# Optimization experiments

Measured on AMD Instinct MI355X. Metric: run time of the kernel, lower is better.

The kernel has to match this reference:

```python
import jax, jax.numpy as jnp
import numpy as np

WIN = 7                 # skimage default win_size (gaussian_weights=False)
K1, K2 = 0.01, 0.03     # skimage defaults
DATA_RANGE = 2.0        # skimage dtype range for float images: dmax - dmin = 1 - (-1)


def _uniform_filter_valid(x):
    """7x7 uniform (mean) filter, VALID padding, depthwise over channels.
    x: [B, C, H, W] -> [B, C, H-6, W-6]. Equivalent to skimage uniform_filter
    followed by crop(pad) since reflected borders are discarded."""
    C = x.shape[1]
    k = jnp.full((C, 1, WIN, WIN), 1.0 / (WIN * WIN), dtype=x.dtype)
    return jax.lax.conv_general_dilated(
        x, k, window_strides=(1, 1), padding='VALID',
        dimension_numbers=('NCHW', 'OIHW', 'NCHW'),
        feature_group_count=C)


def _ssim_mean(pred, target):
    N = WIN * WIN
    cov_norm = N / (N - 1.0)  # sample covariance (skimage use_sample_covariance=True)
    ux = _uniform_filter_valid(pred)
    uy = _uniform_filter_valid(target)
    uxx = _uniform_filter_valid(pred * pred)
    uyy = _uniform_filter_valid(target * target)
    uxy = _uniform_filter_valid(pred * target)
    vx = cov_norm * (uxx - ux * ux)
    vy = cov_norm * (uyy - uy * uy)
    vxy = cov_norm * (uxy - ux * uy)
    C1 = (K1 * DATA_RANGE) ** 2
    C2 = (K2 * DATA_RANGE) ** 2
    S = ((2.0 * ux * uy + C1) * (2.0 * vxy + C2)) / (
        (ux * ux + uy * uy + C1) * (vx + vy + C2))
    # equal-weight mean over channels / images == global mean of valid map
    return jnp.mean(S)


def setup_inputs() -> dict:
    key = jax.random.key(0)
    k1, k2 = jax.random.split(key)
    shape = (32, 3, 512, 512)
    pred = jax.random.uniform(k1, shape, dtype=jnp.float32)
    target = jax.random.uniform(k2, shape, dtype=jnp.float32)
    return {"pred": pred, "target": target}


def reference(pred, target):
    return 1.0 - _ssim_mean(pred, target)
```

## Files before the change

kernel.cpp:

```cpp
#include <hip/hip_runtime.h>

#define IMG 512
#define VALID 506
#define NPLANES 96
#define BAND_ROWS 64
#define NBANDS 8
#define HSTRIDE 520

__device__ __forceinline__ float ssim_val(const float s[5]) {
    const float inv_n = 1.0f / 49.0f;
    const float cn    = 49.0f / 48.0f;
    const float C1 = 4.0e-4f;
    const float C2 = 3.6e-3f;
    float ux  = s[0] * inv_n;
    float uy  = s[1] * inv_n;
    float uxx = s[2] * inv_n;
    float uyy = s[3] * inv_n;
    float uxy = s[4] * inv_n;
    float vx  = cn * (uxx - ux * ux);
    float vy  = cn * (uyy - uy * uy);
    float vxy = cn * (uxy - ux * uy);
    float num = (2.0f * ux * uy + C1) * (2.0f * vxy + C2);
    float den = (ux * ux + uy * uy + C1) * (vx + vy + C2);
    return __fdividef(num, den);
}

__global__ __launch_bounds__(256) void ssim_slide_kernel(
    const float* __restrict__ pred,
    const float* __restrict__ target,
    double* __restrict__ accum)
{
    __shared__ float hv[2][5][HSTRIDE];
    __shared__ float wsum[4];

    const int band  = blockIdx.x;
    const int plane = blockIdx.y;
    const int t = threadIdx.x;
    const int c = t << 1;
    const int b = band * BAND_ROWS;
    const int n = (VALID - b < BAND_ROWS) ? (VALID - b) : BAND_ROWS;

    const float* __restrict__ px_ptr = pred   + (size_t)plane * (IMG * IMG) + c;
    const float* __restrict__ py_ptr = target + (size_t)plane * (IMG * IMG) + c;

    float2 Vx  = make_float2(0.f, 0.f);
    float2 Vy  = Vx, Vxx = Vx, Vyy = Vx, Vxy = Vx;
    float2 hx[7], hy[7];

    #pragma unroll
    for (int k = 0; k < 6; ++k) {
        float2 px = *reinterpret_cast<const float2*>(px_ptr + (size_t)(b + k) * IMG);
        float2 py = *reinterpret_cast<const float2*>(py_ptr + (size_t)(b + k) * IMG);
        hx[k] = px; hy[k] = py;
        Vx.x  += px.x;        Vx.y  += px.y;
        Vy.x  += py.x;        Vy.y  += py.y;
        Vxx.x += px.x * px.x; Vxx.y += px.y * px.y;
        Vyy.x += py.x * py.x; Vyy.y += py.y * py.y;
        Vxy.x += px.x * py.x; Vxy.y += px.y * py.y;
    }

    float local = 0.f;

    auto row_step = [&](float2& hxs, float2& hys, bool do_sub, int r, int p) {
        float2 px = *reinterpret_cast<const float2*>(px_ptr + (size_t)r * IMG);
        float2 py = *reinterpret_cast<const float2*>(py_ptr + (size_t)r * IMG);
        if (do_sub) {
            float2 ox = hxs, oy = hys;
            Vx.x  -= ox.x;        Vx.y  -= ox.y;
            Vy.x  -= oy.x;        Vy.y  -= oy.y;
            Vxx.x -= ox.x * ox.x; Vxx.y -= ox.y * ox.y;
            Vyy.x -= oy.x * oy.x; Vyy.y -= oy.y * oy.y;
            Vxy.x -= ox.x * oy.x; Vxy.y -= ox.y * oy.y;
        }
        hxs = px; hys = py;
        Vx.x  += px.x;        Vx.y  += px.y;
        Vy.x  += py.x;        Vy.y  += py.y;
        Vxx.x += px.x * px.x; Vxx.y += px.y * px.y;
        Vyy.x += py.x * py.x; Vyy.y += py.y * py.y;
        Vxy.x += px.x * py.x; Vxy.y += px.y * py.y;

        *reinterpret_cast<float2*>(&hv[p][0][c]) = Vx;
        *reinterpret_cast<float2*>(&hv[p][1][c]) = Vy;
        *reinterpret_cast<float2*>(&hv[p][2][c]) = Vxx;
        *reinterpret_cast<float2*>(&hv[p][3][c]) = Vyy;
        *reinterpret_cast<float2*>(&hv[p][4][c]) = Vxy;
        __syncthreads();

        if (c < VALID) {
            float s0[5], s1[5];
            #pragma unroll
            for (int m = 0; m < 5; ++m) {
                const float* row = &hv[p][m][c];
                float2 r0 = *reinterpret_cast<const float2*>(row);
                float2 r1 = *reinterpret_cast<const float2*>(row + 2);
                float2 r2 = *reinterpret_cast<const float2*>(row + 4);
                float2 r3 = *reinterpret_cast<const float2*>(row + 6);
                float a = r0.x + r0.y + r1.x + r1.y + r2.x + r2.y + r3.x;
                s0[m] = a;
                s1[m] = a - r0.x + r3.y;
            }
            local += ssim_val(s0);
            local += ssim_val(s1);
        }
    };

    row_step(hx[6], hy[6], false, b + 6, 0);

    for (int ii = 1; ii < BAND_ROWS; ii += 7) {
        #pragma unroll
        for (int k = 0; k < 7; ++k) {
            const int i = ii + k;
            if (i < n)
                row_step(hx[k], hy[k], true, b + 6 + i, i & 1);
        }
    }

    #pragma unroll
    for (int off = 32; off > 0; off >>= 1)
        local += __shfl_down(local, off, 64);
    if ((t & 63) == 0) wsum[t >> 6] = local;
    __syncthreads();
    if (t == 0)
        atomicAdd(accum, (double)(wsum[0] + wsum[1] + wsum[2] + wsum[3]));
}

__global__ void ssim_finalize_kernel(const double* __restrict__ accum,
                                     float* __restrict__ out)
{
    const double n_valid = (double)NPLANES * (double)VALID * (double)VALID;
    out[0] = (float)(1.0 - accum[0] / n_valid);
}

extern "C" void kernel_launch(void* const* d_in, const int* in_sizes, int n_in,
                              void* d_out, int out_size, void* d_ws, size_t ws_size,
                              hipStream_t stream) {
    const float* pred   = (const float*)d_in[0];
    const float* target = (const float*)d_in[1];
    float* out = (float*)d_out;
    double* accum = (double*)d_ws;

    hipMemsetAsync(d_ws, 0, sizeof(double), stream);

    dim3 grid(NBANDS, NPLANES);
    ssim_slide_kernel<<<grid, 256, 0, stream>>>(pred, target, accum);
    ssim_finalize_kernel<<<1, 1, 0, stream>>>(accum, out);
}
```

Measured before the change: 88.29 us.

## Replace shared-memory horizontal sums with per-wave cross-lane permutes in SSIM

Each wavefront now owns a 16-row band covering a whole 512-column row, with each lane holding 8 columns. The horizontal 7-tap sums are done with ds_bpermute from the neighbouring lane instead of going through shared memory, which removes the per-row __syncthreads. Rows leaving the window are reloaded from global memory rather than kept in registers, and the SSIM formula is rescaled algebraically to avoid the 1/49 multiplies. This adds redundant global reads (an extra 6-row halo per band plus the old-row reloads) in exchange for no block-level barriers and more bands available for parallelism.

Result: faster. 82.53 us (-6.5%).

```diff
diff --git a/kernel.cpp b/kernel.cpp
--- a/kernel.cpp
+++ b/kernel.cpp
@@ -1,124 +1,145 @@
 #include <hip/hip_runtime.h>
 
-#define IMG 512
-#define VALID 506
+#define IMG     512
+#define VALID   506
 #define NPLANES 96
-#define BAND_ROWS 64
-#define NBANDS 8
-#define HSTRIDE 520
+#define R       16
+#define BANDS   32
 
-__device__ __forceinline__ float ssim_val(const float s[5]) {
-    const float inv_n = 1.0f / 49.0f;
-    const float cn    = 49.0f / 48.0f;
-    const float C1 = 4.0e-4f;
-    const float C2 = 3.6e-3f;
-    float ux  = s[0] * inv_n;
-    float uy  = s[1] * inv_n;
-    float uxx = s[2] * inv_n;
-    float uyy = s[3] * inv_n;
-    float uxy = s[4] * inv_n;
-    float vx  = cn * (uxx - ux * ux);
-    float vy  = cn * (uyy - uy * uy);
-    float vxy = cn * (uxy - ux * uy);
-    float num = (2.0f * ux * uy + C1) * (2.0f * vxy + C2);
-    float den = (ux * ux + uy * uy + C1) * (vx + vy + C2);
-    return __fdividef(num, den);
+__device__ __forceinline__ float shfl_next(float v, int baddr) {
+    return __int_as_float(__builtin_amdgcn_ds_bpermute(baddr, __float_as_int(v)));
 }
 
-__global__ __launch_bounds__(256) void ssim_slide_kernel(
+__device__ __forceinline__ void addv(float4& V, const float4 p) {
+    V.x += p.x; V.y += p.y; V.z += p.z; V.w += p.w;
+}
+__device__ __forceinline__ void subv(float4& V, const float4 p) {
+    V.x -= p.x; V.y -= p.y; V.z -= p.z; V.w -= p.w;
+}
+__device__ __forceinline__ void addmul(float4& V, const float4 p, const float4 q) {
+    V.x = fmaf(p.x, q.x, V.x); V.y = fmaf(p.y, q.y, V.y);
+    V.z = fmaf(p.z, q.z, V.z); V.w = fmaf(p.w, q.w, V.w);
+}
+__device__ __forceinline__ void submul(float4& V, const float4 p, const float4 q) {
+    V.x = fmaf(-p.x, q.x, V.x); V.y = fmaf(-p.y, q.y, V.y);
+    V.z = fmaf(-p.z, q.z, V.z); V.w = fmaf(-p.w, q.w, V.w);
+}
+
+__device__ __forceinline__ void hsum7(const float4 A, const float4 B, int baddr, float o[8]) {
+    float n0 = shfl_next(A.x, baddr);
+    float n1 = shfl_next(A.y, baddr);
+    float n2 = shfl_next(A.z, baddr);
+    float n3 = shfl_next(A.w, baddr);
+    float n4 = shfl_next(B.x, baddr);
+    float n5 = shfl_next(B.y, baddr);
+    o[0] = ((A.x + A.y) + (A.z + A.w)) + ((B.x + B.y) + B.z);
+    o[1] = (o[0] - A.x) + B.w;
+    o[2] = (o[1] - A.y) + n0;
+    o[3] = (o[2] - A.z) + n1;
+    o[4] = (o[3] - A.w) + n2;
+    o[5] = (o[4] - B.x) + n3;
+    o[6] = (o[5] - B.y) + n4;
+    o[7] = (o[6] - B.z) + n5;
+}
+
+#define LOADROW(x0, x1, y0, y1, r) do {                                         \
+    const float4* _p = reinterpret_cast<const float4*>(pp + (size_t)(r) * IMG); \
+    const float4* _q = reinterpret_cast<const float4*>(pt + (size_t)(r) * IMG); \
+    x0 = _p[0]; x1 = _p[1]; y0 = _q[0]; y1 = _q[1]; } while (0)
+
+__global__ __launch_bounds__(256, 3) void ssim_wave_kernel(
     const float* __restrict__ pred,
     const float* __restrict__ target,
     double* __restrict__ accum)
 {
-    __shared__ float hv[2][5][HSTRIDE];
     __shared__ float wsum[4];
 
-    const int band  = blockIdx.x;
+    const int t     = threadIdx.x;
+    const int lane  = t & 63;
+    const int wv    = t >> 6;
+    const int band  = blockIdx.x * 4 + wv;
     const int plane = blockIdx.y;
-    const int t = threadIdx.x;
-    const int c = t << 1;
-    const int b = band * BAND_ROWS;
-    const int n = (VALID - b < BAND_ROWS) ? (VALID - b) : BAND_ROWS;
+    const int row0  = band * R;
+    const int col   = lane << 3;
 
-    const float* __restrict__ px_ptr = pred   + (size_t)plane * (IMG * IMG) + c;
-    const float* __restrict__ py_ptr = target + (size_t)plane * (IMG * IMG) + c;
+    const size_t pbase = (size_t)plane * (IMG * IMG);
+    const float* __restrict__ pp = pred   + pbase + col;
+    const float* __restrict__ pt = target + pbase + col;
 
-    float2 Vx  = make_float2(0.f, 0.f);
-    float2 Vy  = Vx, Vxx = Vx, Vyy = Vx, Vxy = Vx;
-    float2 hx[7], hy[7];
+    const int baddr = ((lane + 1) & 63) << 2;
 
-    #pragma unroll
+    float4 z = make_float4(0.f, 0.f, 0.f, 0.f);
+    float4 Vx_a = z, Vx_b = z, Vy_a = z, Vy_b = z;
+    float4 Vxx_a = z, Vxx_b = z, Vyy_a = z, Vyy_b = z, Vxy_a = z, Vxy_b = z;
+
+    float4 nx0, nx1, ny0, ny1;
+    LOADROW(nx0, nx1, ny0, ny1, row0);
+
+    #pragma unroll 2
     for (int k = 0; k < 6; ++k) {
-        float2 px = *reinterpret_cast<const float2*>(px_ptr + (size_t)(b + k) * IMG);
-        float2 py = *reinterpret_cast<const float2*>(py_ptr + (size_t)(b + k) * IMG);
-        hx[k] = px; hy[k] = py;
-        Vx.x  += px.x;        Vx.y  += px.y;
-        Vy.x  += py.x;        Vy.y  += py.y;
-        Vxx.x += px.x * px.x; Vxx.y += px.y * px.y;
-        Vyy.x += py.x * py.x; Vyy.y += py.y * py.y;
-        Vxy.x += px.x * py.x; Vxy.y += px.y * py.y;
+        float4 px0 = nx0, px1 = nx1, py0 = ny0, py1 = ny1;
+        LOADROW(nx0, nx1, ny0, ny1, row0 + k + 1);
+        addv(Vx_a, px0);  addv(Vx_b, px1);
+        addv(Vy_a, py0);  addv(Vy_b, py1);
+        addmul(Vxx_a, px0, px0); addmul(Vxx_b, px1, px1);
+        addmul(Vyy_a, py0, py0); addmul(Vyy_b, py1, py1);
+        addmul(Vxy_a, px0, py0); addmul(Vxy_b, px1, py1);
     }
 
+    const float c1 = 0.9604f;
+    const float c2 = 8.4672f;
     float local = 0.f;
 
-    auto row_step = [&](float2& hxs, float2& hys, bool do_sub, int r, int p) {
-        float2 px = *reinterpret_cast<const float2*>(px_ptr + (size_t)r * IMG);
-        float2 py = *reinterpret_cast<const float2*>(py_ptr + (size_t)r * IMG);
-        if (do_sub) {
-            float2 ox = hxs, oy = hys;
-            Vx.x  -= ox.x;        Vx.y  -= ox.y;
-            Vy.x  -= oy.x;        Vy.y  -= oy.y;
-            Vxx.x -= ox.x * ox.x; Vxx.y -= ox.y * ox.y;
-            Vyy.x -= oy.x * oy.x; Vyy.y -= oy.y * oy.y;
-            Vxy.x -= ox.x * oy.x; Vxy.y -= ox.y * oy.y;
+    #pragma unroll 2
+    for (int i = 0; i < R; ++i) {
+        float4 px0 = nx0, px1 = nx1, py0 = ny0, py1 = ny1;
+
+        float4 ox0, ox1, oy0, oy1;
+        const bool has_old = (i > 0);
+        if (has_old) LOADROW(ox0, ox1, oy0, oy1, row0 + i - 1);
+
+        int rn = row0 + 7 + i; rn = rn < IMG - 1 ? rn : IMG - 1;
+        LOADROW(nx0, nx1, ny0, ny1, rn);
+
+        addv(Vx_a, px0);  addv(Vx_b, px1);
+        addv(Vy_a, py0);  addv(Vy_b, py1);
+        addmul(Vxx_a, px0, px0); addmul(Vxx_b, px1, px1);
+        addmul(Vyy_a, py0, py0); addmul(Vyy_b, py1, py1);
+        addmul(Vxy_a, px0, py0); addmul(Vxy_b, px1, py1);
+        if (has_old) {
+            subv(Vx_a, ox0);  subv(Vx_b, ox1);
+            subv(Vy_a, oy0);  subv(Vy_b, oy1);
+            submul(Vxx_a, ox0, ox0); submul(Vxx_b, ox1, ox1);
+            submul(Vyy_a, oy0, oy0); submul(Vyy_b, oy1, oy1);
+            submul(Vxy_a, ox0, oy0); submul(Vxy_b, ox1, oy1);
         }
-        hxs = px; hys = py;
-        Vx.x  += px.x;        Vx.y  += px.y;
-        Vy.x  += py.x;        Vy.y  += py.y;
-        Vxx.x += px.x * px.x; Vxx.y += px.y * px.y;
-        Vyy.x += py.x * py.x; Vyy.y += py.y * py.y;
-        Vxy.x += px.x * py.x; Vxy.y += px.y * py.y;
 
-        *reinterpret_cast<float2*>(&hv[p][0][c]) = Vx;
-        *reinterpret_cast<float2*>(&hv[p][1][c]) = Vy;
-        *reinterpret_cast<float2*>(&hv[p][2][c]) = Vxx;
-        *reinterpret_cast<float2*>(&hv[p][3][c]) = Vyy;
-        *reinterpret_cast<float2*>(&hv[p][4][c]) = Vxy;
-        __syncthreads();
-
-        if (c < VALID) {
-            float s0[5], s1[5];
+        const bool row_ok = (row0 + i) < VALID;
+        if (row_ok) {
+            float hx[8], hy[8], hxx[8], hyy[8], hxy[8];
+            hsum7(Vx_a,  Vx_b,  baddr, hx);
+            hsum7(Vy_a,  Vy_b,  baddr, hy);
+            hsum7(Vxx_a, Vxx_b, baddr, hxx);
+            hsum7(Vyy_a, Vyy_b, baddr, hyy);
+            hsum7(Vxy_a, Vxy_b, baddr, hxy);
             #pragma unroll
-            for (int m = 0; m < 5; ++m) {
-                const float* row = &hv[p][m][c];
-                float2 r0 = *reinterpret_cast<const float2*>(row);
-                float2 r1 = *reinterpret_cast<const float2*>(row + 2);
-                float2 r2 = *reinterpret_cast<const float2*>(row + 4);
-                float2 r3 = *reinterpret_cast<const float2*>(row + 6);
-                float a = r0.x + r0.y + r1.x + r1.y + r2.x + r2.y + r3.x;
-                s0[m] = a;
-                s1[m] = a - r0.x + r3.y;
+            for (int j = 0; j < 8; ++j) {
+                float t1 = hx[j] * hy[j];
+                float t2 = fmaf(hx[j], hx[j], hy[j] * hy[j]);
+                float n1 = fmaf(2.f, t1, c1);
+                float d1 = t2 + c1;
+                float n2 = fmaf(-2.f, t1, fmaf(98.f, hxy[j], c2));
+                float d2 = fmaf(49.f, hxx[j] + hyy[j], c2) - t2;
+                float S  = __fdividef(n1 * n2, d1 * d2);
+                local += (col + j < VALID) ? S : 0.f;
             }
-            local += ssim_val(s0);
-            local += ssim_val(s1);
-        }
-    };
-
-    row_step(hx[6], hy[6], false, b + 6, 0);
-
-    for (int ii = 1; ii < BAND_ROWS; ii += 7) {
-        #pragma unroll
-        for (int k = 0; k < 7; ++k) {
-            const int i = ii + k;
-            if (i < n)
-                row_step(hx[k], hy[k], true, b + 6 + i, i & 1);
         }
     }
 
     #pragma unroll
     for (int off = 32; off > 0; off >>= 1)
         local += __shfl_down(local, off, 64);
-    if ((t & 63) == 0) wsum[t >> 6] = local;
+    if (lane == 0) wsum[wv] = local;
     __syncthreads();
     if (t == 0)
         atomicAdd(accum, (double)(wsum[0] + wsum[1] + wsum[2] + wsum[3]));
@@ -141,7 +162,7 @@
 
     hipMemsetAsync(d_ws, 0, sizeof(double), stream);
 
-    dim3 grid(NBANDS, NPLANES);
-    ssim_slide_kernel<<<grid, 256, 0, stream>>>(pred, target, accum);
+    dim3 grid(BANDS / 4, NPLANES);
+    ssim_wave_kernel<<<grid, 256, 0, stream>>>(pred, target, accum);
     ssim_finalize_kernel<<<1, 1, 0, stream>>>(accum, out);
 }
```
